# Kernel optimization log

Hardware: AMD Instinct MI355X
Metric: run time of the kernel (lower is better)

## Reference

```python
import jax, jax.numpy as jnp
import numpy as np

BOUNDS = 1.6  # aabb = [[b,b,b],[-b,-b,-b]]
C = 72       # output_coordinate_dim per plane


def _sample_planes(grids, coords):
    """Bilinear grid_sample, align_corners=True, padding_mode='border'.
    grids:  [P, C, H, W]
    coords: [P, N, 2] with (x, y) in [-1, 1]; x indexes W, y indexes H.
    returns [P, N, C]
    """
    P, Cc, H, W = grids.shape
    x = (coords[..., 0] + 1.0) * 0.5 * (W - 1)
    y = (coords[..., 1] + 1.0) * 0.5 * (H - 1)
    # border padding: clamp the sampling coordinate to the valid range
    x = jnp.clip(x, 0.0, W - 1)
    y = jnp.clip(y, 0.0, H - 1)
    x0 = jnp.floor(x)
    y0 = jnp.floor(y)
    wx = (x - x0)[..., None]  # [P, N, 1]
    wy = (y - y0)[..., None]
    x0i = x0.astype(jnp.int32)
    y0i = y0.astype(jnp.int32)
    x1i = jnp.minimum(x0i + 1, W - 1)
    y1i = jnp.minimum(y0i + 1, H - 1)

    def one_plane(g, y0i, y1i, x0i, x1i):
        # g: [C, H, W]; index tensors: [N] -> each gather [C, N] -> [N, C]
        v00 = g[:, y0i, x0i].T
        v01 = g[:, y0i, x1i].T
        v10 = g[:, y1i, x0i].T
        v11 = g[:, y1i, x1i].T
        return v00, v01, v10, v11

    v00, v01, v10, v11 = jax.vmap(one_plane)(grids, y0i, y1i, x0i, x1i)
    top = v00 * (1.0 - wx) + v01 * wx
    bot = v10 * (1.0 - wx) + v11 * wx
    return top * (1.0 - wy) + bot * wy  # [P, N, C]


def _triplane_forward(pts, grids_list):
    N = pts.shape[0]
    # normalize_aabb with aabb = [[b,b,b],[-b,-b,-b]]
    pts_n = (pts - BOUNDS) * (2.0 / (-BOUNDS - BOUNDS)) - 1.0  # == -pts / BOUNDS
    # plane coordinate combos: (0,1), (0,2), (1,2)
    coords = jnp.stack([pts_n[:, jnp.array([0, 1])],
                        pts_n[:, jnp.array([0, 2])],
                        pts_n[:, jnp.array([1, 2])]], axis=0)  # [3, N, 2]
    feats = []
    prev = None
    for g in grids_list:  # fixed small loop over scales
        samp = _sample_planes(g, coords)                 # [3, N, C]
        tri = samp.transpose(1, 0, 2).reshape(N, 3 * C)  # concat plane feats
        prev = tri if prev is None else tri + prev       # cumulative across scales
        feats.append(prev)
    return jnp.concatenate(feats, axis=-1)  # [N, 3*C*n_scales]


def setup_inputs() -> dict:
    key = jax.random.key(0)
    ks = jax.random.split(key, 5)
    N = 100000
    pts = jax.random.normal(ks[0], (N, 3), dtype=jnp.float32)
    resos = [64, 128, 256, 512]
    grids = {}
    for i, r in enumerate(resos):
        # original init is uniform(-0.01, 0.01)
        grids[f"grids_s{i}"] = jax.random.uniform(
            ks[i + 1], (3, C, r, r), dtype=jnp.float32, minval=-0.01, maxval=0.01)
    return {"pts": pts, **grids}


def reference(pts, grids_s0, grids_s1, grids_s2, grids_s3):
    return _triplane_forward(pts, [grids_s0, grids_s1, grids_s2, grids_s3])
```

## Files before the change

### kernel.cpp

```cpp
#include <hip/hip_runtime.h>


#define TP_C 72
#define TP_PLANES 3
#define TP_SCALES 4
#define TP_INV_BOUNDS 0.625f
#define TP_CVEC (TP_C / 4)

#define TP_TILES0 96
#define TP_TILES1 480
#define TP_TILES2 2016
#define TP_TILES3 8160

__global__ __launch_bounds__(256) void transpose_all_kernel(
    const float* __restrict__ g0, const float* __restrict__ g1,
    const float* __restrict__ g2, const float* __restrict__ g3,
    float* __restrict__ t0, float* __restrict__ t1,
    float* __restrict__ t2, float* __restrict__ t3)
{
    int b = blockIdx.x;
    const float* in;
    float* out;
    int rr, tile;
    if (b < TP_TILES0)      { in = g0; out = t0; rr = 64 * 64;   tile = b; }
    else if (b < TP_TILES1) { in = g1; out = t1; rr = 128 * 128; tile = b - TP_TILES0; }
    else if (b < TP_TILES2) { in = g2; out = t2; rr = 256 * 256; tile = b - TP_TILES1; }
    else                    { in = g3; out = t3; rr = 512 * 512; tile = b - TP_TILES2; }

    int P0  = tile * 128;
    int p   = P0 / rr;
    int px0 = P0 - p * rr;

    __shared__ float lds[TP_C * 129];

    const float* inp = in + ((size_t)p * TP_C) * (size_t)rr + px0;
    int t = threadIdx.x;

    #pragma unroll
    for (int j = 0; j < 9; ++j) {
        int idx = j * 256 + t;
        int c   = idx >> 5;
        int q4  = idx & 31;
        float4 v = *(const float4*)(inp + (size_t)c * rr + q4 * 4);
        float* l = lds + c * 129 + q4 * 4;
        l[0] = v.x; l[1] = v.y; l[2] = v.z; l[3] = v.w;
    }
    __syncthreads();

    float* outp = out + (size_t)P0 * TP_C;
    #pragma unroll
    for (int j = 0; j < 9; ++j) {
        int idx = j * 256 + t;
        int q   = idx / 18;
        int c4  = idx - q * 18;
        const float* l = lds + (c4 * 4) * 129 + q;
        float4 v;
        v.x = l[0 * 129];
        v.y = l[1 * 129];
        v.z = l[2 * 129];
        v.w = l[3 * 129];
        *(float4*)(outp + (size_t)idx * 4) = v;
    }
}

__global__ __launch_bounds__(256) void triplane_gather_kernel(
    const float* __restrict__ pts,
    const float* __restrict__ t0,
    const float* __restrict__ t1,
    const float* __restrict__ t2,
    const float* __restrict__ t3,
    float* __restrict__ out,
    int N)
{
    int idx = blockIdx.x * blockDim.x + threadIdx.x;
    int total = N * TP_PLANES * TP_CVEC;
    if (idx >= total) return;

    int cv = idx % TP_CVEC;
    int t  = idx / TP_CVEC;
    int p  = t % TP_PLANES;
    int n  = t / TP_PLANES;

    float nx = -pts[n * 3 + 0] * TP_INV_BOUNDS;
    float ny = -pts[n * 3 + 1] * TP_INV_BOUNDS;
    float nz = -pts[n * 3 + 2] * TP_INV_BOUNDS;

    float cx, cy;
    if (p == 0)      { cx = nx; cy = ny; }
    else if (p == 1) { cx = nx; cy = nz; }
    else             { cx = ny; cy = nz; }

    const float* grids[TP_SCALES] = { t0, t1, t2, t3 };
    const int    res[TP_SCALES]   = { 64, 128, 256, 512 };

    float4 acc = make_float4(0.f, 0.f, 0.f, 0.f);
    float* outrow = out + (size_t)n * (TP_SCALES * TP_PLANES * TP_C)
                        + (size_t)p * TP_C + cv * 4;

    #pragma unroll
    for (int s = 0; s < TP_SCALES; ++s) {
        const int r = res[s];
        const float rm1 = (float)(r - 1);

        float fx = (cx + 1.0f) * 0.5f * rm1;
        float fy = (cy + 1.0f) * 0.5f * rm1;
        fx = fminf(fmaxf(fx, 0.0f), rm1);
        fy = fminf(fmaxf(fy, 0.0f), rm1);

        float x0f = floorf(fx);
        float y0f = floorf(fy);
        float wx = fx - x0f;
        float wy = fy - y0f;
        int x0 = (int)x0f;
        int y0 = (int)y0f;
        int x1 = min(x0 + 1, r - 1);
        int y1 = min(y0 + 1, r - 1);

        const float* g = grids[s] + ((size_t)p * r * r) * TP_C + (size_t)cv * 4;
        const float4* r0c0 = (const float4*)(g + ((size_t)y0 * r + x0) * TP_C);
        const float4* r0c1 = (const float4*)(g + ((size_t)y0 * r + x1) * TP_C);
        const float4* r1c0 = (const float4*)(g + ((size_t)y1 * r + x0) * TP_C);
        const float4* r1c1 = (const float4*)(g + ((size_t)y1 * r + x1) * TP_C);

        float4 v00 = *r0c0;
        float4 v01 = *r0c1;
        float4 v10 = *r1c0;
        float4 v11 = *r1c1;

        float iwx = 1.0f - wx;
        float iwy = 1.0f - wy;

        float tpx, tpy, tpz, tpw, bt;
        tpx = v00.x * iwx + v01.x * wx;
        bt  = v10.x * iwx + v11.x * wx;
        acc.x += tpx * iwy + bt * wy;
        tpy = v00.y * iwx + v01.y * wx;
        bt  = v10.y * iwx + v11.y * wx;
        acc.y += tpy * iwy + bt * wy;
        tpz = v00.z * iwx + v01.z * wx;
        bt  = v10.z * iwx + v11.z * wx;
        acc.z += tpz * iwy + bt * wy;
        tpw = v00.w * iwx + v01.w * wx;
        bt  = v10.w * iwx + v11.w * wx;
        acc.w += tpw * iwy + bt * wy;

        *(float4*)(outrow + s * (TP_PLANES * TP_C)) = acc;
    }
}

extern "C" void kernel_launch(void* const* d_in, const int* in_sizes, int n_in,
                              void* d_out, int out_size, void* d_ws, size_t ws_size,
                              hipStream_t stream) {
    const float* pts = (const float*)d_in[0];
    const float* g[TP_SCALES] = {
        (const float*)d_in[1], (const float*)d_in[2],
        (const float*)d_in[3], (const float*)d_in[4] };
    float* out = (float*)d_out;

    const int res[TP_SCALES] = { 64, 128, 256, 512 };

    float* tg[TP_SCALES];
    size_t off = 0;
    for (int s = 0; s < TP_SCALES; ++s) {
        tg[s] = (float*)d_ws + off;
        off += (size_t)TP_PLANES * TP_C * res[s] * res[s];
    }

    transpose_all_kernel<<<TP_TILES3, 256, 0, stream>>>(
        g[0], g[1], g[2], g[3], tg[0], tg[1], tg[2], tg[3]);

    int N = in_sizes[0] / 3;
    int total = N * TP_PLANES * TP_CVEC;
    int block = 256;
    int grid = (total + block - 1) / block;
    triplane_gather_kernel<<<grid, block, 0, stream>>>(
        pts, tg[0], tg[1], tg[2], tg[3], out, N);
}
```

Measured before the change: 765.4 us.

## Sort points by Morton key before gathering; use nontemporal loads/stores

Adds a counting-sort pipeline (key histogram, prefix scan, scatter) that orders points by a 15-bit Morton code, so neighbouring threads in the gather kernel sample nearby grid texels and share cache lines. The transpose uses nontemporal loads and the gather output uses nontemporal stores to limit cache pollution. The cost is three extra small kernels plus a memset, atomics on the histogram, and scattered output writes from the permuted order.

Measured after the change: 726.3 us. 1.05x faster.

```diff
diff --git a/kernel.cpp b/kernel.cpp
--- a/kernel.cpp
+++ b/kernel.cpp
@@ -7,10 +7,14 @@
 #define TP_INV_BOUNDS 0.625f
 #define TP_CVEC (TP_C / 4)
 
+typedef float tp_f4 __attribute__((ext_vector_type(4)));
+
 #define TP_TILES0 96
 #define TP_TILES1 480
 #define TP_TILES2 2016
 #define TP_TILES3 8160
+
+#define TP_NBINS 32768
 
 __global__ __launch_bounds__(256) void transpose_all_kernel(
     const float* __restrict__ g0, const float* __restrict__ g1,
@@ -41,7 +45,8 @@
         int idx = j * 256 + t;
         int c   = idx >> 5;
         int q4  = idx & 31;
-        float4 v = *(const float4*)(inp + (size_t)c * rr + q4 * 4);
+        tp_f4 v = __builtin_nontemporal_load(
+            (const tp_f4*)(inp + (size_t)c * rr + q4 * 4));
         float* l = lds + c * 129 + q4 * 4;
         l[0] = v.x; l[1] = v.y; l[2] = v.z; l[3] = v.w;
     }
@@ -63,8 +68,69 @@
     }
 }
 
+__device__ __forceinline__ unsigned tp_expand5(unsigned v) {
+    unsigned r = (v & 1);
+    r |= (v & 2)  << 2;
+    r |= (v & 4)  << 4;
+    r |= (v & 8)  << 6;
+    r |= (v & 16) << 8;
+    return r;
+}
+
+__global__ __launch_bounds__(256) void keys_kernel(
+    const float* __restrict__ pts, unsigned* __restrict__ keys,
+    unsigned* __restrict__ hist, int N)
+{
+    int n = blockIdx.x * 256 + threadIdx.x;
+    if (n >= N) return;
+    float nx = fminf(fmaxf(-pts[n * 3 + 0] * TP_INV_BOUNDS, -1.f), 1.f);
+    float ny = fminf(fmaxf(-pts[n * 3 + 1] * TP_INV_BOUNDS, -1.f), 1.f);
+    float nz = fminf(fmaxf(-pts[n * 3 + 2] * TP_INV_BOUNDS, -1.f), 1.f);
+    int qx = min(31, max(0, (int)((nx + 1.f) * 16.f)));
+    int qy = min(31, max(0, (int)((ny + 1.f) * 16.f)));
+    int qz = min(31, max(0, (int)((nz + 1.f) * 16.f)));
+    unsigned key = tp_expand5((unsigned)qx)
+                 | (tp_expand5((unsigned)qy) << 1)
+                 | (tp_expand5((unsigned)qz) << 2);
+    keys[n] = key;
+    atomicAdd(&hist[key], 1u);
+}
+
+__global__ __launch_bounds__(1024) void prefix_kernel(
+    const unsigned* __restrict__ hist, unsigned* __restrict__ binoff)
+{
+    __shared__ unsigned part[1024];
+    int t = threadIdx.x;
+    unsigned local[32];
+    unsigned s = 0;
+    #pragma unroll
+    for (int i = 0; i < 32; ++i) { local[i] = hist[t * 32 + i]; s += local[i]; }
+    part[t] = s;
+    __syncthreads();
+    for (int off = 1; off < 1024; off <<= 1) {
+        unsigned v = (t >= off) ? part[t - off] : 0u;
+        __syncthreads();
+        part[t] += v;
+        __syncthreads();
+    }
+    unsigned run = (t == 0) ? 0u : part[t - 1];
+    #pragma unroll
+    for (int i = 0; i < 32; ++i) { binoff[t * 32 + i] = run; run += local[i]; }
+}
+
+__global__ __launch_bounds__(256) void scatter_kernel(
+    const unsigned* __restrict__ keys, unsigned* __restrict__ binoff,
+    unsigned* __restrict__ perm, int N)
+{
+    int n = blockIdx.x * 256 + threadIdx.x;
+    if (n >= N) return;
+    unsigned pos = atomicAdd(&binoff[keys[n]], 1u);
+    perm[pos] = n;
+}
+
 __global__ __launch_bounds__(256) void triplane_gather_kernel(
     const float* __restrict__ pts,
+    const unsigned* __restrict__ perm,
     const float* __restrict__ t0,
     const float* __restrict__ t1,
     const float* __restrict__ t2,
@@ -79,7 +145,8 @@
     int cv = idx % TP_CVEC;
     int t  = idx / TP_CVEC;
     int p  = t % TP_PLANES;
-    int n  = t / TP_PLANES;
+    int ns = t / TP_PLANES;
+    int n  = (int)perm[ns];
 
     float nx = -pts[n * 3 + 0] * TP_INV_BOUNDS;
     float ny = -pts[n * 3 + 1] * TP_INV_BOUNDS;
@@ -117,34 +184,31 @@
         int y1 = min(y0 + 1, r - 1);
 
         const float* g = grids[s] + ((size_t)p * r * r) * TP_C + (size_t)cv * 4;
-        const float4* r0c0 = (const float4*)(g + ((size_t)y0 * r + x0) * TP_C);
-        const float4* r0c1 = (const float4*)(g + ((size_t)y0 * r + x1) * TP_C);
-        const float4* r1c0 = (const float4*)(g + ((size_t)y1 * r + x0) * TP_C);
-        const float4* r1c1 = (const float4*)(g + ((size_t)y1 * r + x1) * TP_C);
-
-        float4 v00 = *r0c0;
-        float4 v01 = *r0c1;
-        float4 v10 = *r1c0;
-        float4 v11 = *r1c1;
+        float4 v00 = *(const float4*)(g + ((size_t)y0 * r + x0) * TP_C);
+        float4 v01 = *(const float4*)(g + ((size_t)y0 * r + x1) * TP_C);
+        float4 v10 = *(const float4*)(g + ((size_t)y1 * r + x0) * TP_C);
+        float4 v11 = *(const float4*)(g + ((size_t)y1 * r + x1) * TP_C);
 
         float iwx = 1.0f - wx;
         float iwy = 1.0f - wy;
 
-        float tpx, tpy, tpz, tpw, bt;
-        tpx = v00.x * iwx + v01.x * wx;
+        float tp0, bt;
+        tp0 = v00.x * iwx + v01.x * wx;
         bt  = v10.x * iwx + v11.x * wx;
-        acc.x += tpx * iwy + bt * wy;
-        tpy = v00.y * iwx + v01.y * wx;
+        acc.x += tp0 * iwy + bt * wy;
+        tp0 = v00.y * iwx + v01.y * wx;
         bt  = v10.y * iwx + v11.y * wx;
-        acc.y += tpy * iwy + bt * wy;
-        tpz = v00.z * iwx + v01.z * wx;
+        acc.y += tp0 * iwy + bt * wy;
+        tp0 = v00.z * iwx + v01.z * wx;
         bt  = v10.z * iwx + v11.z * wx;
-        acc.z += tpz * iwy + bt * wy;
-        tpw = v00.w * iwx + v01.w * wx;
+        acc.z += tp0 * iwy + bt * wy;
+        tp0 = v00.w * iwx + v01.w * wx;
         bt  = v10.w * iwx + v11.w * wx;
-        acc.w += tpw * iwy + bt * wy;
-
-        *(float4*)(outrow + s * (TP_PLANES * TP_C)) = acc;
+        acc.w += tp0 * iwy + bt * wy;
+
+        tp_f4 av = { acc.x, acc.y, acc.z, acc.w };
+        __builtin_nontemporal_store(av,
+            (tp_f4*)(outrow + s * (TP_PLANES * TP_C)));
     }
 }
 
@@ -158,21 +222,35 @@
     float* out = (float*)d_out;
 
     const int res[TP_SCALES] = { 64, 128, 256, 512 };
-
+    int N = in_sizes[0] / 3;
+
+    unsigned* hist   = (unsigned*)d_ws;
+    unsigned* binoff = hist + TP_NBINS;
+    unsigned* keys   = binoff + TP_NBINS;
+    unsigned* perm   = keys + N;
+    size_t meta = (size_t)2 * TP_NBINS + (size_t)2 * N;
+    meta = (meta + 3) & ~(size_t)3;
     float* tg[TP_SCALES];
-    size_t off = 0;
+    size_t off = meta;
     for (int s = 0; s < TP_SCALES; ++s) {
         tg[s] = (float*)d_ws + off;
         off += (size_t)TP_PLANES * TP_C * res[s] * res[s];
     }
 
+    (void)hipMemsetAsync(hist, 0, TP_NBINS * sizeof(unsigned), stream);
+
+    int pblocks = (N + 255) / 256;
+    keys_kernel<<<pblocks, 256, 0, stream>>>(pts, keys, hist, N);
+
     transpose_all_kernel<<<TP_TILES3, 256, 0, stream>>>(
         g[0], g[1], g[2], g[3], tg[0], tg[1], tg[2], tg[3]);
 
-    int N = in_sizes[0] / 3;
+    prefix_kernel<<<1, 1024, 0, stream>>>(hist, binoff);
+    scatter_kernel<<<pblocks, 256, 0, stream>>>(keys, binoff, perm, N);
+
     int total = N * TP_PLANES * TP_CVEC;
     int block = 256;
     int grid = (total + block - 1) / block;
     triplane_gather_kernel<<<grid, block, 0, stream>>>(
-        pts, tg[0], tg[1], tg[2], tg[3], out, N);
-}
+        pts, perm, tg[0], tg[1], tg[2], tg[3], out, N);
+}
```
